# Performance work log

Hardware: AMD Instinct MI355X
Metric: run time of the kernel (lower is better)

The kernel has to match this reference:

```python
import jax, jax.numpy as jnp
import numpy as np

EPS = 1e-05
MARGIN = 0.0


def setup_inputs() -> dict:
    key = jax.random.key(0)
    k1, k2 = jax.random.split(key)
    embeddings = jax.random.normal(k1, (512, 512), dtype=jnp.float32)
    labels = jax.random.randint(k2, (512,), 0, 32, dtype=jnp.int64)
    return {"embeddings": embeddings, "labels": labels}


def _pairwise_distance(e, squared=False):
    # e: [B, D] -> [B, B] euclidean distances
    dot = jnp.matmul(e, e.T)
    sq = jnp.diag(dot)
    d = sq[:, None] - 2.0 * dot + sq[None, :]
    d = jnp.maximum(d, 0.0)
    if not squared:
        zmask = (d == 0.0).astype(d.dtype)
        d = d + zmask * EPS
        d = jnp.sqrt(d) + EPS
        d = d * (1.0 - zmask)
    return d


def _triplet_mask(labels):
    B = labels.shape[0]
    not_eq = ~jnp.eye(B, dtype=bool)
    # distinct indices i != j, i != k, j != k  -> [B, B, B]
    distinct = not_eq[:, :, None] & not_eq[:, None, :] & not_eq[None, :, :]
    lab_eq = labels[None, :] == labels[:, None]  # symmetric [B, B]
    valid = lab_eq[:, :, None] & (~lab_eq[:, None, :])  # label[i]==label[j], label[i]!=label[k]
    return (distinct & valid).astype(jnp.float32)


def reference(embeddings, labels):
    d = _pairwise_distance(embeddings, squared=False)  # [B, B]
    # triplet_loss[a, p, n] = d[a, p] - d[a, n] + margin
    tl = d[:, :, None] - d[:, None, :] + MARGIN
    mask = _triplet_mask(labels)
    tl = jnp.maximum(mask * tl, 0.0)
    num_positive = jnp.sum((tl > 1e-05).astype(jnp.float32))
    num_valid = jnp.sum(mask)
    fraction_positive = num_positive / (num_valid + 1e-05)
    loss = jnp.sum(tl) / (num_positive + 1e-05)
    return (loss, fraction_positive)
```

## Files before the change

kernel.cpp:

```cpp
#include <hip/hip_runtime.h>

#define BSZ 512
#define EPSF 1e-5f
#define KT   64
#define NS   8
#define TT   64
#define LSTR 68

#define WS_PARTIAL 8
#define WS_P       2048

__device__ __forceinline__ float dist_xform(float v) {
    v = fmaxf(v, 0.0f);
    float z = (v == 0.0f) ? 1.0f : 0.0f;
    v = sqrtf(v + z * EPSF) + EPSF;
    return v * (1.0f - z);
}

__global__ __launch_bounds__(256) void dsq_kernel(const float* __restrict__ E,
                                                  float* __restrict__ ws) {
    __shared__ __align__(16) float As[KT][LSTR];
    __shared__ __align__(16) float Bs[KT][LSTR];
    const int tid = threadIdx.x;
    const int bj = blockIdx.x * TT;
    const int bi = blockIdx.y * TT;
    const int k0 = blockIdx.z * KT;

    {
        const int r0 = tid >> 4;
        const int kc = (tid & 15) * 4;
#pragma unroll
        for (int p = 0; p < 4; ++p) {
            const int row = p * 16 + r0;
            float4 va = *(const float4*)(E + (size_t)(bi + row) * BSZ + k0 + kc);
            float4 vb = *(const float4*)(E + (size_t)(bj + row) * BSZ + k0 + kc);
            As[kc  ][row] = va.x; As[kc+1][row] = va.y; As[kc+2][row] = va.z; As[kc+3][row] = va.w;
            Bs[kc  ][row] = vb.x; Bs[kc+1][row] = vb.y; Bs[kc+2][row] = vb.z; Bs[kc+3][row] = vb.w;
        }
    }
    __syncthreads();

    const int tx = tid & 15;
    const int ty = tid >> 4;
    float acc[4][4];
#pragma unroll
    for (int r = 0; r < 4; ++r)
#pragma unroll
        for (int c = 0; c < 4; ++c) acc[r][c] = 0.0f;

#pragma unroll 8
    for (int kk = 0; kk < KT; ++kk) {
        float4 A0 = *(const float4*)&As[kk][ty * 4];
        float4 B0 = *(const float4*)&Bs[kk][tx * 4];
        float ar[4] = {A0.x, A0.y, A0.z, A0.w};
        float br[4] = {B0.x, B0.y, B0.z, B0.w};
#pragma unroll
        for (int r = 0; r < 4; ++r)
#pragma unroll
            for (int c = 0; c < 4; ++c) {
                float d = ar[r] - br[c];
                acc[r][c] = fmaf(d, d, acc[r][c]);
            }
    }

    float* Pp = ws + WS_P + (size_t)blockIdx.z * BSZ * BSZ;
#pragma unroll
    for (int r = 0; r < 4; ++r) {
        float4 v = {acc[r][0], acc[r][1], acc[r][2], acc[r][3]};
        *(float4*)(Pp + (size_t)(bi + ty * 4 + r) * BSZ + bj + tx * 4) = v;
    }
}

__global__ __launch_bounds__(256) void triplet_kernel(const int* __restrict__ labels,
                                                      const float* __restrict__ ws,
                                                      float* __restrict__ partial) {
    const int a = blockIdx.x;
    const int tid = threadIdx.x;
    __shared__ float drow[BSZ];
    __shared__ int   lab[BSZ];
    __shared__ int   poslist[BSZ];
    __shared__ int   npos_s;
    __shared__ float wsum[4];
    __shared__ int   wcnt[4];

    if (tid == 0) npos_s = 0;
    for (int t = tid; t < BSZ; t += 256) lab[t] = labels[t];

    const float* P = ws + WS_P;
    {
        float2 s2 = {0.f, 0.f};
#pragma unroll
        for (int s = 0; s < NS; ++s) {
            float2 v = *(const float2*)(P + ((size_t)s * BSZ + a) * BSZ + tid * 2);
            s2.x += v.x; s2.y += v.y;
        }
        drow[tid * 2 + 0] = dist_xform(s2.x);
        drow[tid * 2 + 1] = dist_xform(s2.y);
    }
    __syncthreads();

    const int la = lab[a];
    for (int t = tid; t < BSZ; t += 256) {
        if (lab[t] == la && t != a) {
            int idx = atomicAdd(&npos_s, 1);
            poslist[idx] = t;
        }
    }
    __syncthreads();

    const int npos = npos_s;
    const int nneg = BSZ - 1 - npos;
    float sum = 0.0f;
    int   cnt = 0;
    const int total = npos * BSZ;
    for (int idx = tid; idx < total; idx += 256) {
        const int p = poslist[idx >> 9];
        const int n = idx & (BSZ - 1);
        if (lab[n] != la) {
            const float v = drow[p] - drow[n];
            if (v > 0.0f)  sum += v;
            if (v > 1e-5f) cnt++;
        }
    }
#pragma unroll
    for (int off = 32; off > 0; off >>= 1) {
        sum += __shfl_down(sum, off);
        cnt += __shfl_down(cnt, off);
    }
    const int wave = tid >> 6, lane = tid & 63;
    if (lane == 0) { wsum[wave] = sum; wcnt[wave] = cnt; }
    __syncthreads();
    if (tid == 0) {
        partial[a]           = wsum[0] + wsum[1] + wsum[2] + wsum[3];
        partial[BSZ + a]     = (float)(wcnt[0] + wcnt[1] + wcnt[2] + wcnt[3]);
        partial[2*BSZ + a]   = (float)npos * (float)nneg;
    }
}

__global__ __launch_bounds__(256) void final_kernel(const float* __restrict__ partial,
                                                    float* __restrict__ out) {
    const int tid = threadIdx.x;
    float s = partial[tid]         + partial[tid + 256];
    float c = partial[BSZ + tid]   + partial[BSZ + tid + 256];
    float v = partial[2*BSZ + tid] + partial[2*BSZ + tid + 256];
#pragma unroll
    for (int off = 32; off > 0; off >>= 1) {
        s += __shfl_down(s, off);
        c += __shfl_down(c, off);
        v += __shfl_down(v, off);
    }
    __shared__ float ws_[4], wc[4], wv[4];
    const int wave = tid >> 6, lane = tid & 63;
    if (lane == 0) { ws_[wave] = s; wc[wave] = c; wv[wave] = v; }
    __syncthreads();
    if (tid == 0) {
        float S = ws_[0] + ws_[1] + ws_[2] + ws_[3];
        float C = wc[0] + wc[1] + wc[2] + wc[3];
        float V = wv[0] + wv[1] + wv[2] + wv[3];
        out[0] = S / (C + 1e-5f);
        out[1] = C / (V + 1e-5f);
    }
}

extern "C" void kernel_launch(void* const* d_in, const int* in_sizes, int n_in,
                              void* d_out, int out_size, void* d_ws, size_t ws_size,
                              hipStream_t stream) {
    const float* E      = (const float*)d_in[0];
    const int*   labels = (const int*)d_in[1];
    float* out = (float*)d_out;
    float* ws  = (float*)d_ws;
    float* partial = ws + WS_PARTIAL;

    dsq_kernel<<<dim3(8, 8, NS), 256, 0, stream>>>(E, ws);
    triplet_kernel<<<BSZ, 256, 0, stream>>>(labels, ws, partial);
    final_kernel<<<1, 256, 0, stream>>>(partial, out);
}
```

Measured before the change: 79.16 us.

## Fuse distance, triplet and final reduction into one kernel with last-block finish

```diff
diff --git a/kernel.cpp b/kernel.cpp
--- a/kernel.cpp
+++ b/kernel.cpp
@@ -1,14 +1,11 @@
 #include <hip/hip_runtime.h>
 
-#define BSZ 512
+#define BSZ  512
 #define EPSF 1e-5f
-#define KT   64
-#define NS   8
-#define TT   64
-#define LSTR 68
+#define NBLK 256
+#define NTHR 512
 
 #define WS_PARTIAL 8
-#define WS_P       2048
 
 __device__ __forceinline__ float dist_xform(float v) {
     v = fmaxf(v, 0.0f);
@@ -17,148 +14,117 @@
     return v * (1.0f - z);
 }
 
-__global__ __launch_bounds__(256) void dsq_kernel(const float* __restrict__ E,
-                                                  float* __restrict__ ws) {
-    __shared__ __align__(16) float As[KT][LSTR];
-    __shared__ __align__(16) float Bs[KT][LSTR];
-    const int tid = threadIdx.x;
-    const int bj = blockIdx.x * TT;
-    const int bi = blockIdx.y * TT;
-    const int k0 = blockIdx.z * KT;
-
-    {
-        const int r0 = tid >> 4;
-        const int kc = (tid & 15) * 4;
-#pragma unroll
-        for (int p = 0; p < 4; ++p) {
-            const int row = p * 16 + r0;
-            float4 va = *(const float4*)(E + (size_t)(bi + row) * BSZ + k0 + kc);
-            float4 vb = *(const float4*)(E + (size_t)(bj + row) * BSZ + k0 + kc);
-            As[kc  ][row] = va.x; As[kc+1][row] = va.y; As[kc+2][row] = va.z; As[kc+3][row] = va.w;
-            Bs[kc  ][row] = vb.x; Bs[kc+1][row] = vb.y; Bs[kc+2][row] = vb.z; Bs[kc+3][row] = vb.w;
-        }
-    }
-    __syncthreads();
-
-    const int tx = tid & 15;
-    const int ty = tid >> 4;
-    float acc[4][4];
-#pragma unroll
-    for (int r = 0; r < 4; ++r)
-#pragma unroll
-        for (int c = 0; c < 4; ++c) acc[r][c] = 0.0f;
-
-#pragma unroll 8
-    for (int kk = 0; kk < KT; ++kk) {
-        float4 A0 = *(const float4*)&As[kk][ty * 4];
-        float4 B0 = *(const float4*)&Bs[kk][tx * 4];
-        float ar[4] = {A0.x, A0.y, A0.z, A0.w};
-        float br[4] = {B0.x, B0.y, B0.z, B0.w};
-#pragma unroll
-        for (int r = 0; r < 4; ++r)
-#pragma unroll
-            for (int c = 0; c < 4; ++c) {
-                float d = ar[r] - br[c];
-                acc[r][c] = fmaf(d, d, acc[r][c]);
-            }
-    }
-
-    float* Pp = ws + WS_P + (size_t)blockIdx.z * BSZ * BSZ;
-#pragma unroll
-    for (int r = 0; r < 4; ++r) {
-        float4 v = {acc[r][0], acc[r][1], acc[r][2], acc[r][3]};
-        *(float4*)(Pp + (size_t)(bi + ty * 4 + r) * BSZ + bj + tx * 4) = v;
-    }
-}
-
-__global__ __launch_bounds__(256) void triplet_kernel(const int* __restrict__ labels,
-                                                      const float* __restrict__ ws,
-                                                      float* __restrict__ partial) {
-    const int a = blockIdx.x;
-    const int tid = threadIdx.x;
+__global__ __launch_bounds__(NTHR) void fused_kernel(const float* __restrict__ E,
+                                                     const int* __restrict__ labels,
+                                                     float* __restrict__ ws,
+                                                     float* __restrict__ out) {
+    __shared__ __align__(16) float ea0[BSZ];
+    __shared__ __align__(16) float ea1[BSZ];
     __shared__ float drow[BSZ];
     __shared__ int   lab[BSZ];
     __shared__ int   poslist[BSZ];
     __shared__ int   npos_s;
-    __shared__ float wsum[4];
-    __shared__ int   wcnt[4];
+    __shared__ float wsum[8];
+    __shared__ int   wcnt[8];
+    __shared__ float fs[4], fc[4], fv[4];
+    __shared__ unsigned rank_s;
 
-    if (tid == 0) npos_s = 0;
-    for (int t = tid; t < BSZ; t += 256) lab[t] = labels[t];
+    const int tid = threadIdx.x;
+    const int a0  = blockIdx.x * 2;
+    float* partial = ws + WS_PARTIAL;
 
-    const float* P = ws + WS_P;
-    {
-        float2 s2 = {0.f, 0.f};
+    lab[tid] = labels[tid];
+    ea0[tid] = E[(size_t)a0 * BSZ + tid];
+    ea1[tid] = E[(size_t)(a0 + 1) * BSZ + tid];
+    __syncthreads();
+
+    float acc0a = 0.f, acc0b = 0.f, acc1a = 0.f, acc1b = 0.f;
+    const float4* rj = (const float4*)(E + (size_t)tid * BSZ);
+#pragma unroll 8
+    for (int k4 = 0; k4 < BSZ / 4; ++k4) {
+        const float4 x  = rj[k4];
+        const float4 e0 = *(const float4*)&ea0[k4 * 4];
+        const float4 e1 = *(const float4*)&ea1[k4 * 4];
+        float d;
+        d = x.x - e0.x; acc0a = fmaf(d, d, acc0a);
+        d = x.y - e0.y; acc0b = fmaf(d, d, acc0b);
+        d = x.z - e0.z; acc0a = fmaf(d, d, acc0a);
+        d = x.w - e0.w; acc0b = fmaf(d, d, acc0b);
+        d = x.x - e1.x; acc1a = fmaf(d, d, acc1a);
+        d = x.y - e1.y; acc1b = fmaf(d, d, acc1b);
+        d = x.z - e1.z; acc1a = fmaf(d, d, acc1a);
+        d = x.w - e1.w; acc1b = fmaf(d, d, acc1b);
+    }
+
+    auto do_anchor = [&](int a, float acc) {
+        if (tid == 0) npos_s = 0;
+        drow[tid] = dist_xform(acc);
+        __syncthreads();
+
+        const int la = lab[a];
+        if (lab[tid] == la && tid != a) poslist[atomicAdd(&npos_s, 1)] = tid;
+        __syncthreads();
+
+        const int   npos = npos_s;
+        const float dn   = drow[tid];
+        float sum = 0.f; int cnt = 0;
+        if (lab[tid] != la) {
+            for (int m = 0; m < npos; ++m) {
+                const float v = drow[poslist[m]] - dn;
+                if (v > 0.f)    sum += v;
+                if (v > 1e-5f)  cnt++;
+            }
+        }
 #pragma unroll
-        for (int s = 0; s < NS; ++s) {
-            float2 v = *(const float2*)(P + ((size_t)s * BSZ + a) * BSZ + tid * 2);
-            s2.x += v.x; s2.y += v.y;
+        for (int off = 32; off > 0; off >>= 1) {
+            sum += __shfl_down(sum, off);
+            cnt += __shfl_down(cnt, off);
         }
-        drow[tid * 2 + 0] = dist_xform(s2.x);
-        drow[tid * 2 + 1] = dist_xform(s2.y);
+        const int wave = tid >> 6, lane = tid & 63;
+        if (lane == 0) { wsum[wave] = sum; wcnt[wave] = cnt; }
+        __syncthreads();
+        if (tid == 0) {
+            float S = 0.f; int C = 0;
+#pragma unroll
+            for (int w = 0; w < 8; ++w) { S += wsum[w]; C += wcnt[w]; }
+            partial[a]            = S;
+            partial[BSZ + a]      = (float)C;
+            partial[2 * BSZ + a]  = (float)npos * (float)(BSZ - 1 - npos);
+        }
+        __syncthreads();
+    };
+    do_anchor(a0,     acc0a + acc0b);
+    do_anchor(a0 + 1, acc1a + acc1b);
+
+    if (tid == 0) {
+        __threadfence();
+        rank_s = atomicAdd((unsigned*)ws, 1u);
     }
     __syncthreads();
-
-    const int la = lab[a];
-    for (int t = tid; t < BSZ; t += 256) {
-        if (lab[t] == la && t != a) {
-            int idx = atomicAdd(&npos_s, 1);
-            poslist[idx] = t;
+    if ((rank_s & (NBLK - 1)) == NBLK - 1) {
+        __threadfence();
+        if (tid < 256) {
+            volatile const float* vp = partial;
+            float s = vp[tid]           + vp[tid + 256];
+            float c = vp[BSZ + tid]     + vp[BSZ + tid + 256];
+            float v = vp[2*BSZ + tid]   + vp[2*BSZ + tid + 256];
+#pragma unroll
+            for (int off = 32; off > 0; off >>= 1) {
+                s += __shfl_down(s, off);
+                c += __shfl_down(c, off);
+                v += __shfl_down(v, off);
+            }
+            const int wave = tid >> 6, lane = tid & 63;
+            if (lane == 0) { fs[wave] = s; fc[wave] = c; fv[wave] = v; }
         }
-    }
-    __syncthreads();
-
-    const int npos = npos_s;
-    const int nneg = BSZ - 1 - npos;
-    float sum = 0.0f;
-    int   cnt = 0;
-    const int total = npos * BSZ;
-    for (int idx = tid; idx < total; idx += 256) {
-        const int p = poslist[idx >> 9];
-        const int n = idx & (BSZ - 1);
-        if (lab[n] != la) {
-            const float v = drow[p] - drow[n];
-            if (v > 0.0f)  sum += v;
-            if (v > 1e-5f) cnt++;
+        __syncthreads();
+        if (tid == 0) {
+            const float S = fs[0] + fs[1] + fs[2] + fs[3];
+            const float C = fc[0] + fc[1] + fc[2] + fc[3];
+            const float V = fv[0] + fv[1] + fv[2] + fv[3];
+            out[0] = S / (C + 1e-5f);
+            out[1] = C / (V + 1e-5f);
         }
-    }
-#pragma unroll
-    for (int off = 32; off > 0; off >>= 1) {
-        sum += __shfl_down(sum, off);
-        cnt += __shfl_down(cnt, off);
-    }
-    const int wave = tid >> 6, lane = tid & 63;
-    if (lane == 0) { wsum[wave] = sum; wcnt[wave] = cnt; }
-    __syncthreads();
-    if (tid == 0) {
-        partial[a]           = wsum[0] + wsum[1] + wsum[2] + wsum[3];
-        partial[BSZ + a]     = (float)(wcnt[0] + wcnt[1] + wcnt[2] + wcnt[3]);
-        partial[2*BSZ + a]   = (float)npos * (float)nneg;
-    }
-}
-
-__global__ __launch_bounds__(256) void final_kernel(const float* __restrict__ partial,
-                                                    float* __restrict__ out) {
-    const int tid = threadIdx.x;
-    float s = partial[tid]         + partial[tid + 256];
-    float c = partial[BSZ + tid]   + partial[BSZ + tid + 256];
-    float v = partial[2*BSZ + tid] + partial[2*BSZ + tid + 256];
-#pragma unroll
-    for (int off = 32; off > 0; off >>= 1) {
-        s += __shfl_down(s, off);
-        c += __shfl_down(c, off);
-        v += __shfl_down(v, off);
-    }
-    __shared__ float ws_[4], wc[4], wv[4];
-    const int wave = tid >> 6, lane = tid & 63;
-    if (lane == 0) { ws_[wave] = s; wc[wave] = c; wv[wave] = v; }
-    __syncthreads();
-    if (tid == 0) {
-        float S = ws_[0] + ws_[1] + ws_[2] + ws_[3];
-        float C = wc[0] + wc[1] + wc[2] + wc[3];
-        float V = wv[0] + wv[1] + wv[2] + wv[3];
-        out[0] = S / (C + 1e-5f);
-        out[1] = C / (V + 1e-5f);
     }
 }
 
@@ -169,9 +135,6 @@
     const int*   labels = (const int*)d_in[1];
     float* out = (float*)d_out;
     float* ws  = (float*)d_ws;
-    float* partial = ws + WS_PARTIAL;
 
-    dsq_kernel<<<dim3(8, 8, NS), 256, 0, stream>>>(E, ws);
-    triplet_kernel<<<BSZ, 256, 0, stream>>>(labels, ws, partial);
-    final_kernel<<<1, 256, 0, stream>>>(partial, out);
+    fused_kernel<<<NBLK, NTHR, 0, stream>>>(E, labels, ws, out);
 }
```

After: 93.26 us. 1.18x slower.

## Switch to dot-product Gram form, two anchors per block, fuse final reduction via atomics

Applied to the files above, without the earlier changes.

```diff
diff --git a/kernel.cpp b/kernel.cpp
--- a/kernel.cpp
+++ b/kernel.cpp
@@ -6,9 +6,11 @@
 #define NS   8
 #define TT   64
 #define LSTR 68
-
-#define WS_PARTIAL 8
-#define WS_P       2048
+#define NBLK2 256
+
+#define WS_ACC 16
+#define WS_SQ  4096
+#define WS_P   8192
 
 __device__ __forceinline__ float dist_xform(float v) {
     v = fmaxf(v, 0.0f);
@@ -17,14 +19,22 @@
     return v * (1.0f - z);
 }
 
-__global__ __launch_bounds__(256) void dsq_kernel(const float* __restrict__ E,
-                                                  float* __restrict__ ws) {
+__global__ __launch_bounds__(256) void dsq_dot_kernel(const float* __restrict__ E,
+                                                      float* __restrict__ ws) {
     __shared__ __align__(16) float As[KT][LSTR];
     __shared__ __align__(16) float Bs[KT][LSTR];
     const int tid = threadIdx.x;
-    const int bj = blockIdx.x * TT;
-    const int bi = blockIdx.y * TT;
-    const int k0 = blockIdx.z * KT;
+    const int bx = blockIdx.x, by = blockIdx.y, bz = blockIdx.z;
+    const int bj = bx * TT;
+    const int bi = by * TT;
+    const int k0 = bz * KT;
+
+    if (tid == 0 && bx == 0 && by == 0 && bz == 0) {
+        ws[WS_ACC + 0] = 0.0f;
+        ws[WS_ACC + 1] = 0.0f;
+        ws[WS_ACC + 2] = 0.0f;
+        ((unsigned*)ws)[WS_ACC + 3] = 0u;
+    }
 
     {
         const int r0 = tid >> 4;
@@ -57,108 +67,135 @@
 #pragma unroll
         for (int r = 0; r < 4; ++r)
 #pragma unroll
-            for (int c = 0; c < 4; ++c) {
-                float d = ar[r] - br[c];
-                acc[r][c] = fmaf(d, d, acc[r][c]);
-            }
-    }
-
-    float* Pp = ws + WS_P + (size_t)blockIdx.z * BSZ * BSZ;
+            for (int c = 0; c < 4; ++c)
+                acc[r][c] = fmaf(ar[r], br[c], acc[r][c]);
+    }
+
+    float* Gp = ws + WS_P + (size_t)bz * BSZ * BSZ;
 #pragma unroll
     for (int r = 0; r < 4; ++r) {
         float4 v = {acc[r][0], acc[r][1], acc[r][2], acc[r][3]};
-        *(float4*)(Pp + (size_t)(bi + ty * 4 + r) * BSZ + bj + tx * 4) = v;
-    }
-}
-
-__global__ __launch_bounds__(256) void triplet_kernel(const int* __restrict__ labels,
-                                                      const float* __restrict__ ws,
-                                                      float* __restrict__ partial) {
-    const int a = blockIdx.x;
+        *(float4*)(Gp + (size_t)(bi + ty * 4 + r) * BSZ + bj + tx * 4) = v;
+    }
+
+    if (bx == by && tx == ty) {
+#pragma unroll
+        for (int r = 0; r < 4; ++r)
+            ws[WS_SQ + (size_t)bz * BSZ + bi + ty * 4 + r] = acc[r][r];
+    }
+}
+
+__global__ __launch_bounds__(256) void triplet2_kernel(const int* __restrict__ labels,
+                                                       float* __restrict__ ws,
+                                                       float* __restrict__ out) {
+    const int b = blockIdx.x;
     const int tid = threadIdx.x;
-    __shared__ float drow[BSZ];
+    const int a0 = 2 * b, a1 = 2 * b + 1;
+    __shared__ float drow0[BSZ];
+    __shared__ float drow1[BSZ];
+    __shared__ float sql[BSZ];
     __shared__ int   lab[BSZ];
     __shared__ int   poslist[BSZ];
     __shared__ int   npos_s;
     __shared__ float wsum[4];
     __shared__ int   wcnt[4];
 
+    const float* G = ws + WS_P;
+    float2 g0 = {0.f, 0.f}, g1 = {0.f, 0.f}, q = {0.f, 0.f};
+#pragma unroll
+    for (int s = 0; s < NS; ++s) {
+        float2 v0 = *(const float2*)(G + ((size_t)s * BSZ + a0) * BSZ + tid * 2);
+        float2 v1 = *(const float2*)(G + ((size_t)s * BSZ + a1) * BSZ + tid * 2);
+        float2 vq = *(const float2*)(ws + WS_SQ + (size_t)s * BSZ + tid * 2);
+        g0.x += v0.x; g0.y += v0.y;
+        g1.x += v1.x; g1.y += v1.y;
+        q.x  += vq.x; q.y  += vq.y;
+    }
+    lab[tid]       = labels[tid];
+    lab[tid + 256] = labels[tid + 256];
+    sql[2 * tid]     = q.x;
+    sql[2 * tid + 1] = q.y;
     if (tid == 0) npos_s = 0;
-    for (int t = tid; t < BSZ; t += 256) lab[t] = labels[t];
-
-    const float* P = ws + WS_P;
+    __syncthreads();
+
+    const float sqa0 = sql[a0], sqa1 = sql[a1];
+    drow0[2 * tid]     = dist_xform(sqa0 + q.x - 2.0f * g0.x);
+    drow0[2 * tid + 1] = dist_xform(sqa0 + q.y - 2.0f * g0.y);
+    drow1[2 * tid]     = dist_xform(sqa1 + q.x - 2.0f * g1.x);
+    drow1[2 * tid + 1] = dist_xform(sqa1 + q.y - 2.0f * g1.y);
+    __syncthreads();
+
+    float sum_t = 0.0f;
+    int   cnt_t = 0;
+    float Vb    = 0.0f;
+
     {
-        float2 s2 = {0.f, 0.f};
-#pragma unroll
-        for (int s = 0; s < NS; ++s) {
-            float2 v = *(const float2*)(P + ((size_t)s * BSZ + a) * BSZ + tid * 2);
-            s2.x += v.x; s2.y += v.y;
-        }
-        drow[tid * 2 + 0] = dist_xform(s2.x);
-        drow[tid * 2 + 1] = dist_xform(s2.y);
-    }
-    __syncthreads();
-
-    const int la = lab[a];
-    for (int t = tid; t < BSZ; t += 256) {
-        if (lab[t] == la && t != a) {
-            int idx = atomicAdd(&npos_s, 1);
-            poslist[idx] = t;
-        }
-    }
-    __syncthreads();
-
-    const int npos = npos_s;
-    const int nneg = BSZ - 1 - npos;
-    float sum = 0.0f;
-    int   cnt = 0;
-    const int total = npos * BSZ;
-    for (int idx = tid; idx < total; idx += 256) {
-        const int p = poslist[idx >> 9];
-        const int n = idx & (BSZ - 1);
-        if (lab[n] != la) {
-            const float v = drow[p] - drow[n];
-            if (v > 0.0f)  sum += v;
-            if (v > 1e-5f) cnt++;
-        }
-    }
+        const int la = lab[a0];
+        for (int t = tid; t < BSZ; t += 256)
+            if (lab[t] == la && t != a0) poslist[atomicAdd(&npos_s, 1)] = t;
+        __syncthreads();
+        const int npos = npos_s;
+        const int total = npos * BSZ;
+        for (int idx = tid; idx < total; idx += 256) {
+            const int p = poslist[idx >> 9];
+            const int n = idx & (BSZ - 1);
+            if (lab[n] != la) {
+                const float v = drow0[p] - drow0[n];
+                if (v > 0.0f)  sum_t += v;
+                if (v > 1e-5f) cnt_t++;
+            }
+        }
+        if (tid == 0) Vb += (float)npos * (float)(BSZ - 1 - npos);
+        __syncthreads();
+        if (tid == 0) npos_s = 0;
+        __syncthreads();
+    }
+    {
+        const int la = lab[a1];
+        for (int t = tid; t < BSZ; t += 256)
+            if (lab[t] == la && t != a1) poslist[atomicAdd(&npos_s, 1)] = t;
+        __syncthreads();
+        const int npos = npos_s;
+        const int total = npos * BSZ;
+        for (int idx = tid; idx < total; idx += 256) {
+            const int p = poslist[idx >> 9];
+            const int n = idx & (BSZ - 1);
+            if (lab[n] != la) {
+                const float v = drow1[p] - drow1[n];
+                if (v > 0.0f)  sum_t += v;
+                if (v > 1e-5f) cnt_t++;
+            }
+        }
+        if (tid == 0) Vb += (float)npos * (float)(BSZ - 1 - npos);
+    }
+
 #pragma unroll
     for (int off = 32; off > 0; off >>= 1) {
-        sum += __shfl_down(sum, off);
-        cnt += __shfl_down(cnt, off);
+        sum_t += __shfl_down(sum_t, off);
+        cnt_t += __shfl_down(cnt_t, off);
     }
     const int wave = tid >> 6, lane = tid & 63;
-    if (lane == 0) { wsum[wave] = sum; wcnt[wave] = cnt; }
-    __syncthreads();
+    if (lane == 0) { wsum[wave] = sum_t; wcnt[wave] = cnt_t; }
+    __syncthreads();
+
     if (tid == 0) {
-        partial[a]           = wsum[0] + wsum[1] + wsum[2] + wsum[3];
-        partial[BSZ + a]     = (float)(wcnt[0] + wcnt[1] + wcnt[2] + wcnt[3]);
-        partial[2*BSZ + a]   = (float)npos * (float)nneg;
-    }
-}
-
-__global__ __launch_bounds__(256) void final_kernel(const float* __restrict__ partial,
-                                                    float* __restrict__ out) {
-    const int tid = threadIdx.x;
-    float s = partial[tid]         + partial[tid + 256];
-    float c = partial[BSZ + tid]   + partial[BSZ + tid + 256];
-    float v = partial[2*BSZ + tid] + partial[2*BSZ + tid + 256];
-#pragma unroll
-    for (int off = 32; off > 0; off >>= 1) {
-        s += __shfl_down(s, off);
-        c += __shfl_down(c, off);
-        v += __shfl_down(v, off);
-    }
-    __shared__ float ws_[4], wc[4], wv[4];
-    const int wave = tid >> 6, lane = tid & 63;
-    if (lane == 0) { ws_[wave] = s; wc[wave] = c; wv[wave] = v; }
-    __syncthreads();
-    if (tid == 0) {
-        float S = ws_[0] + ws_[1] + ws_[2] + ws_[3];
-        float C = wc[0] + wc[1] + wc[2] + wc[3];
-        float V = wv[0] + wv[1] + wv[2] + wv[3];
-        out[0] = S / (C + 1e-5f);
-        out[1] = C / (V + 1e-5f);
+        const float Sb = wsum[0] + wsum[1] + wsum[2] + wsum[3];
+        const float Cb = (float)(wcnt[0] + wcnt[1] + wcnt[2] + wcnt[3]);
+        float* acc = ws + WS_ACC;
+        float o0 = __hip_atomic_fetch_add(&acc[0], Sb, __ATOMIC_RELAXED, __HIP_MEMORY_SCOPE_AGENT);
+        float o1 = __hip_atomic_fetch_add(&acc[1], Cb, __ATOMIC_RELAXED, __HIP_MEMORY_SCOPE_AGENT);
+        float o2 = __hip_atomic_fetch_add(&acc[2], Vb, __ATOMIC_RELAXED, __HIP_MEMORY_SCOPE_AGENT);
+        asm volatile("" :: "v"(o0), "v"(o1), "v"(o2));
+        asm volatile("s_waitcnt vmcnt(0)" ::: "memory");
+        const unsigned r = __hip_atomic_fetch_add((unsigned*)&acc[3], 1u,
+                                                  __ATOMIC_RELAXED, __HIP_MEMORY_SCOPE_AGENT);
+        if (r == (unsigned)(NBLK2 - 1)) {
+            const float S = __hip_atomic_load(&acc[0], __ATOMIC_RELAXED, __HIP_MEMORY_SCOPE_AGENT);
+            const float C = __hip_atomic_load(&acc[1], __ATOMIC_RELAXED, __HIP_MEMORY_SCOPE_AGENT);
+            const float V = __hip_atomic_load(&acc[2], __ATOMIC_RELAXED, __HIP_MEMORY_SCOPE_AGENT);
+            out[0] = S / (C + 1e-5f);
+            out[1] = C / (V + 1e-5f);
+        }
     }
 }
 
@@ -169,9 +206,7 @@
     const int*   labels = (const int*)d_in[1];
     float* out = (float*)d_out;
     float* ws  = (float*)d_ws;
-    float* partial = ws + WS_PARTIAL;
-
-    dsq_kernel<<<dim3(8, 8, NS), 256, 0, stream>>>(E, ws);
-    triplet_kernel<<<BSZ, 256, 0, stream>>>(labels, ws, partial);
-    final_kernel<<<1, 256, 0, stream>>>(partial, out);
-}
+
+    dsq_dot_kernel<<<dim3(8, 8, NS), 256, 0, stream>>>(E, ws);
+    triplet2_kernel<<<NBLK2, 256, 0, stream>>>(labels, ws, out);
+}
```

Result: slower. 87.77 us (+10.9%).
